# Kernel optimization log

Hardware: AMD Instinct MI355X
Metric: run time of the kernel (lower is better)

Reference implementation:

```python
import jax, jax.numpy as jnp
import numpy as np

B, T, F, G, H, N, C = 32, 64, 32, 32, 256, 20000, 32
EPS = 1e-5


def setup_inputs() -> dict:
    key = jax.random.key(0)
    ks = jax.random.split(key, 24)
    s = 0.05
    d = {}
    d["data_feats"] = jax.random.normal(ks[0], (B, T, F), jnp.float32)
    d["gat_output"] = jax.random.normal(ks[1], (B, N, G), jnp.float32)
    d["row_ids"] = jax.random.randint(ks[2], (B, T), 0, 2 * N, jnp.int32)
    d["node_ids"] = jax.random.randint(ks[3], (N,), 0, 2 * N, jnp.int32)
    # shared LSTM (2 layers): layer0 input F+G, layer1 input H; b = b_ih + b_hh fused
    d["shared_Wih0"] = jax.random.normal(ks[4], (4 * H, F + G)) * s
    d["shared_Whh0"] = jax.random.normal(ks[5], (4 * H, H)) * s
    d["shared_b0"] = jax.random.normal(ks[6], (4 * H,)) * s
    d["shared_Wih1"] = jax.random.normal(ks[7], (4 * H, H)) * s
    d["shared_Whh1"] = jax.random.normal(ks[8], (4 * H, H)) * s
    d["shared_b1"] = jax.random.normal(ks[9], (4 * H,)) * s
    # act/time/timeR LSTMs stacked on leading axis 3, each 2 layers of [4H,H]
    d["heads_Wih"] = jax.random.normal(ks[10], (3, 2, 4 * H, H)) * s
    d["heads_Whh"] = jax.random.normal(ks[11], (3, 2, 4 * H, H)) * s
    d["heads_b"] = jax.random.normal(ks[12], (3, 2, 4 * H)) * s
    d["bn_gnn_g"] = jnp.ones((G,), jnp.float32)
    d["bn_gnn_b"] = jnp.zeros((G,), jnp.float32)
    d["bn_shared_g"] = jnp.ones((H,), jnp.float32)
    d["bn_shared_b"] = jnp.zeros((H,), jnp.float32)
    d["heads_bn_g"] = jnp.ones((3, H), jnp.float32)
    d["heads_bn_b"] = jnp.zeros((3, H), jnp.float32)
    d["fc_act_W"] = jax.random.normal(ks[13], (C, H)) * s
    d["fc_act_b"] = jnp.zeros((C,), jnp.float32)
    d["fc_time_W"] = jax.random.normal(ks[14], (1, H)) * s
    d["fc_time_b"] = jnp.zeros((1,), jnp.float32)
    d["fc_timeR_W"] = jax.random.normal(ks[15], (1, H)) * s
    d["fc_timeR_b"] = jnp.zeros((1,), jnp.float32)
    return d


def batchnorm(x, gamma, beta):
    # BatchNorm1d training-mode: stats over (batch, length) per channel; x: [B, L, C]
    mean = jnp.mean(x, axis=(0, 1))
    var = jnp.var(x, axis=(0, 1))
    return (x - mean) * (gamma / jnp.sqrt(var + EPS)) + beta


def lstm_layer(x, Wih, Whh, b):
    # x: [B, T, Din]; PyTorch gate order i, f, g, o
    xp = jnp.einsum("btf,gf->btg", x, Wih) + b  # [B, T, 4H]
    h = Whh.shape[1]
    init = (jnp.zeros((x.shape[0], h), x.dtype), jnp.zeros((x.shape[0], h), x.dtype))

    def step(carry, xt):
        hprev, cprev = carry
        gates = xt + hprev @ Whh.T
        i, f, g, o = jnp.split(gates, 4, axis=-1)
        c = jax.nn.sigmoid(f) * cprev + jax.nn.sigmoid(i) * jnp.tanh(g)
        hnew = jax.nn.sigmoid(o) * jnp.tanh(c)
        return (hnew, c), hnew

    _, hs = jax.lax.scan(step, init, jnp.swapaxes(xp, 0, 1))
    return jnp.swapaxes(hs, 0, 1)  # [B, T, H]


def reference(data_feats, gat_output, row_ids, node_ids,
              shared_Wih0, shared_Whh0, shared_b0,
              shared_Wih1, shared_Whh1, shared_b1,
              heads_Wih, heads_Whh, heads_b,
              bn_gnn_g, bn_gnn_b, bn_shared_g, bn_shared_b,
              heads_bn_g, heads_bn_b,
              fc_act_W, fc_act_b, fc_time_W, fc_time_b, fc_timeR_W, fc_timeR_b):
    # --- graph branch: BN over GAT output, value-match lookup + gather ---
    gat_norm = batchnorm(gat_output, bn_gnn_g, bn_gnn_b)  # [B, N, G]
    eq = row_ids[:, :, None] == node_ids[None, None, :]   # [B, T, N]
    idx = jnp.argmax(eq, axis=-1)                          # first matching index
    found = jnp.any(eq, axis=-1)
    gathered = jnp.take_along_axis(gat_norm, idx[:, :, None], axis=1)  # [B, T, G]
    matched = jnp.where(found[:, :, None], gathered, 0.0)
    lstm_in = jnp.concatenate([data_feats, matched], axis=-1)  # [B, T, F+G]

    # --- shared 2-layer LSTM + BN (dropout off / eval) ---
    shared = lstm_layer(lstm_in, shared_Wih0, shared_Whh0, shared_b0)
    shared = lstm_layer(shared, shared_Wih1, shared_Whh1, shared_b1)
    shared = batchnorm(shared, bn_shared_g, bn_shared_b)

    # --- act / time / timeR head LSTMs (vmapped over the 3 heads) + BN ---
    def head(Wih, Whh, b, g, bb):
        hh = lstm_layer(shared, Wih[0], Whh[0], b[0])
        hh = lstm_layer(hh, Wih[1], Whh[1], b[1])
        return batchnorm(hh, g, bb)

    heads = jax.vmap(head)(heads_Wih, heads_Whh, heads_b, heads_bn_g, heads_bn_b)
    last = heads[:, :, -1, :]  # [3, B, H]

    act = jax.nn.softmax(last[0] @ fc_act_W.T + fc_act_b, axis=1)
    time = last[1] @ fc_time_W.T + fc_time_b
    timeR = last[2] @ fc_timeR_W.T + fc_timeR_b
    return act, time, timeR
```

## Files before the change

### kernel.cpp

```cpp
#include <hip/hip_runtime.h>
#include <hip/hip_fp16.h>
#include <math.h>

#define Bn 32
#define Tn 64
#define Fdim 32
#define Gdim 32
#define Hdim 256
#define Ndim 20000
#define Cdim 32
#define G4 1024
#define BT 2048
#define EPSc 1e-5f

__device__ __forceinline__ float sigmoidf_(float x){ return 1.0f/(1.0f + __expf(-x)); }
__device__ __forceinline__ float tanhf_(float x){ return 2.0f/(1.0f+__expf(-2.0f*x)) - 1.0f; }

typedef _Float16 h2t __attribute__((ext_vector_type(2)));

__device__ __forceinline__ float fdot2_(unsigned w, unsigned h, float acc){
#if defined(__has_builtin) && __has_builtin(__builtin_amdgcn_fdot2)
  return __builtin_amdgcn_fdot2(__builtin_bit_cast(h2t, w), __builtin_bit_cast(h2t, h), acc, false);
#else
  h2t a = __builtin_bit_cast(h2t, w), b = __builtin_bit_cast(h2t, h);
  acc = fmaf((float)a.x, (float)b.x, acc);
  return fmaf((float)a.y, (float)b.y, acc);
#endif
}

__device__ __forceinline__ unsigned packh_(float lo, float hi){
  unsigned ulo = (unsigned)__half_as_ushort(__float2half(lo));
  unsigned uhi = (unsigned)__half_as_ushort(__float2half(hi));
  return ulo | (uhi << 16);
}

__global__ void init_kernel(float* ws){
  int i = blockIdx.x*256 + threadIdx.x;
  if (i < 2112) ws[i] = 0.0f;
  int* table = (int*)(ws + 2112);
  if (i < 40000) table[i] = 0x7fffffff;
}

__global__ void bn_stats_kernel(const float* __restrict__ gat, float* __restrict__ sums){
  __shared__ float ss[256], sq[256];
  int tid = threadIdx.x;
  int idx = blockIdx.x*256 + tid;
  int stride = gridDim.x*256;
  const int total = Bn*Ndim*Gdim;
  float s=0.f,q=0.f;
  for (int i=idx; i<total; i+=stride){ float v = gat[i]; s+=v; q+=v*v; }
  ss[tid]=s; sq[tid]=q; __syncthreads();
  for (int off=128; off>=32; off>>=1){
    if(tid<off){ ss[tid]+=ss[tid+off]; sq[tid]+=sq[tid+off]; }
    __syncthreads();
  }
  if (tid<32){ atomicAdd(&sums[tid], ss[tid]); atomicAdd(&sums[32+tid], sq[tid]); }
}

__global__ void table_kernel(const int* __restrict__ node_ids, int* __restrict__ table){
  int i = blockIdx.x*256 + threadIdx.x;
  if (i < Ndim) atomicMin(&table[node_ids[i]], i);
}

__global__ void build_input_kernel(const float* __restrict__ feats, const float* __restrict__ gat,
    const int* __restrict__ row_ids, const int* __restrict__ table, const float* __restrict__ sums,
    const float* __restrict__ bng, const float* __restrict__ bnb, unsigned* __restrict__ out){
  int gt = blockIdx.x*256 + threadIdx.x;
  int pos = gt >> 5; int k2 = gt & 31;
  float lo, hi;
  if (k2 < 16){
    float2 v = *(const float2*)(feats + pos*Fdim + 2*k2);
    lo = v.x; hi = v.y;
  } else {
    int g0 = 2*(k2-16);
    int r = row_ids[pos];
    int idx = table[r];
    if (idx < Ndim){
      int b = pos / Tn;
      float2 x = *(const float2*)(gat + (size_t)(b*Ndim + idx)*Gdim + g0);
      const float cnt = (float)(Bn*Ndim);
      float m0 = sums[g0]/cnt,   v0 = sums[32+g0]/cnt - m0*m0;
      float m1 = sums[g0+1]/cnt, v1 = sums[32+g0+1]/cnt - m1*m1;
      lo = (x.x-m0)*bng[g0]*rsqrtf(v0+EPSc) + bnb[g0];
      hi = (x.y-m1)*bng[g0+1]*rsqrtf(v1+EPSc) + bnb[g0+1];
    } else { lo = 0.0f; hi = 0.0f; }
  }
  out[gt] = packh_(lo, hi);
}

struct TArgs { const float* src[8]; unsigned* dst[8]; int K[8]; };
__global__ void packwih_kernel(TArgs a){
  __shared__ unsigned tile[32][33];
  int mat = blockIdx.y;
  int K = a.K[mat];
  int K2 = K >> 1;
  int ktiles = K2 >> 5;
  int tk = blockIdx.x & 3;
  int tn = blockIdx.x >> 2;
  if (tk >= ktiles) return;
  const float* src = a.src[mat];
  unsigned* dst = a.dst[mat];
  int tx = threadIdx.x, ty = threadIdx.y;
  int n0 = tn*32, k2_0 = tk*32;
  #pragma unroll
  for (int i=0;i<4;i++){
    int nn = ty + 8*i;
    const float* p = src + (size_t)(n0+nn)*K + 2*(k2_0 + tx);
    tile[nn][tx] = packh_(p[0], p[1]);
  }
  __syncthreads();
  #pragma unroll
  for (int i=0;i<4;i++){
    int r = ty + 8*i;
    dst[(size_t)(k2_0 + r)*G4 + n0 + tx] = tile[tx][r];
  }
}

struct PkArgs { const float* src[8]; };
__global__ void pack_kernel(PkArgs a, unsigned* __restrict__ dst){
  int gid = blockIdx.x*256 + threadIdx.x;
  int m = gid >> 17;
  int rem = gid & 0x1FFFF;
  int q = rem & 3;
  int t2 = (rem >> 2) & 1023;
  int ci = rem >> 12;
  int c = ci >> 3, i = ci & 7;
  int j = t2 & 255, kq = t2 >> 8;
  int r = 4*j + c;
  int k = kq*64 + 8*i + 2*q;
  const float* W = a.src[m];
  dst[gid] = packh_(W[r*256 + k], W[r*256 + k + 1]);
}

struct PArgs { const unsigned* x[3]; const unsigned* wt[3]; const float* bias[3]; float* out[3]; int K2; };
__global__ __launch_bounds__(256) void proj_kernel(PArgs a){
  int hd = blockIdx.z;
  int n  = blockIdx.y*256 + threadIdx.x;
  int m0 = blockIdx.x*8;
  int K2 = a.K2;
  const unsigned* xh = a.x[hd] + (size_t)m0*K2;
  const unsigned* wt = a.wt[hd];
  float bv = a.bias[hd][n];
  float acc[8];
  #pragma unroll
  for (int i=0;i<8;i++) acc[i]=bv;
  for (int k2=0;k2<K2;k2+=4){
    unsigned w0 = wt[(size_t)(k2+0)*G4+n];
    unsigned w1 = wt[(size_t)(k2+1)*G4+n];
    unsigned w2 = wt[(size_t)(k2+2)*G4+n];
    unsigned w3 = wt[(size_t)(k2+3)*G4+n];
    #pragma unroll
    for (int i=0;i<8;i++){
      uint4 xv = *(const uint4*)(xh + i*K2 + k2);
      acc[i]=fdot2_(w0,xv.x,acc[i]); acc[i]=fdot2_(w1,xv.y,acc[i]);
      acc[i]=fdot2_(w2,xv.z,acc[i]); acc[i]=fdot2_(w3,xv.w,acc[i]);
    }
  }
  float* out = a.out[hd] + (size_t)m0*G4 + n;
  #pragma unroll
  for (int i=0;i<8;i++) out[i*G4]=acc[i];
}

struct RArgs { const float* xp[3]; const unsigned* wt[3]; float* out[3]; unsigned* outh[3]; };
__global__ __launch_bounds__(1024,1) void rec_kernel(RArgs a){
  extern __shared__ float lds[];
  unsigned* lw   = (unsigned*)lds;
  float*    part = lds + 32768;
  unsigned* hp   = (unsigned*)(lds + 36864);
  int b = blockIdx.x, hd = blockIdx.y, tid = threadIdx.x;
  int j = tid & 255, kq = tid >> 8;
  const float* xp = a.xp[hd] + (size_t)b*Tn*G4;
  const unsigned* wt = a.wt[hd];
  float* out = a.out[hd] + (size_t)b*Tn*Hdim;
  unsigned* outh = a.outh[hd] + (size_t)b*Tn*128;

  unsigned w[96];
  #pragma unroll
  for (int c=0;c<4;c++){
    #pragma unroll
    for (int i=0;i<6;i++){
      uint4 v = *(const uint4*)(wt + ((c*8+i)*1024 + tid)*4);
      w[(c*6+i)*4+0]=v.x; w[(c*6+i)*4+1]=v.y; w[(c*6+i)*4+2]=v.z; w[(c*6+i)*4+3]=v.w;
    }
    #pragma unroll
    for (int i=6;i<8;i++){
      uint4 v = *(const uint4*)(wt + ((c*8+i)*1024 + tid)*4);
      *(uint4*)(lw + ((c*2+(i-6))*1024 + tid)*4) = v;
    }
  }
  float cst = 0.0f;
  if (tid < 128){ hp[tid] = 0u; hp[128+tid] = 0u; }
  __syncthreads();

  int p = 0;
  for (int t=0; t<Tn; t++){
    float ac0, ac1, ac2, ac3;
    if (kq == 0){
      float4 xv = *(const float4*)(xp + t*G4 + 4*j);
      ac0=xv.x; ac1=xv.y; ac2=xv.z; ac3=xv.w;
    } else { ac0=0.f; ac1=0.f; ac2=0.f; ac3=0.f; }
    const unsigned* hrow = hp + p*128 + kq*32;
    #pragma unroll
    for (int ic=0; ic<6; ic++){
      uint4 hv = *(const uint4*)(hrow + 4*ic);
      ac0=fdot2_(w[0*24+ic*4+0],hv.x,ac0); ac0=fdot2_(w[0*24+ic*4+1],hv.y,ac0);
      ac0=fdot2_(w[0*24+ic*4+2],hv.z,ac0); ac0=fdot2_(w[0*24+ic*4+3],hv.w,ac0);
      ac1=fdot2_(w[1*24+ic*4+0],hv.x,ac1); ac1=fdot2_(w[1*24+ic*4+1],hv.y,ac1);
      ac1=fdot2_(w[1*24+ic*4+2],hv.z,ac1); ac1=fdot2_(w[1*24+ic*4+3],hv.w,ac1);
      ac2=fdot2_(w[2*24+ic*4+0],hv.x,ac2); ac2=fdot2_(w[2*24+ic*4+1],hv.y,ac2);
      ac2=fdot2_(w[2*24+ic*4+2],hv.z,ac2); ac2=fdot2_(w[2*24+ic*4+3],hv.w,ac2);
      ac3=fdot2_(w[3*24+ic*4+0],hv.x,ac3); ac3=fdot2_(w[3*24+ic*4+1],hv.y,ac3);
      ac3=fdot2_(w[3*24+ic*4+2],hv.z,ac3); ac3=fdot2_(w[3*24+ic*4+3],hv.w,ac3);
    }
    #pragma unroll
    for (int ic=6; ic<8; ic++){
      uint4 hv = *(const uint4*)(hrow + 4*ic);
      { uint4 lv = *(const uint4*)(lw + ((0*2+(ic-6))*1024 + tid)*4);
        ac0=fdot2_(lv.x,hv.x,ac0); ac0=fdot2_(lv.y,hv.y,ac0);
        ac0=fdot2_(lv.z,hv.z,ac0); ac0=fdot2_(lv.w,hv.w,ac0); }
      { uint4 lv = *(const uint4*)(lw + ((1*2+(ic-6))*1024 + tid)*4);
        ac1=fdot2_(lv.x,hv.x,ac1); ac1=fdot2_(lv.y,hv.y,ac1);
        ac1=fdot2_(lv.z,hv.z,ac1); ac1=fdot2_(lv.w,hv.w,ac1); }
      { uint4 lv = *(const uint4*)(lw + ((2*2+(ic-6))*1024 + tid)*4);
        ac2=fdot2_(lv.x,hv.x,ac2); ac2=fdot2_(lv.y,hv.y,ac2);
        ac2=fdot2_(lv.z,hv.z,ac2); ac2=fdot2_(lv.w,hv.w,ac2); }
      { uint4 lv = *(const uint4*)(lw + ((3*2+(ic-6))*1024 + tid)*4);
        ac3=fdot2_(lv.x,hv.x,ac3); ac3=fdot2_(lv.y,hv.y,ac3);
        ac3=fdot2_(lv.z,hv.z,ac3); ac3=fdot2_(lv.w,hv.w,ac3); }
    }
    *(float4*)(part + kq*1024 + 4*j) = make_float4(ac0,ac1,ac2,ac3);
    __syncthreads();
    if (tid < 256){
      int u = tid;
      float gi = part[u]     + part[1024+u]     + part[2048+u]     + part[3072+u];
      float gf = part[256+u] + part[1024+256+u] + part[2048+256+u] + part[3072+256+u];
      float gg = part[512+u] + part[1024+512+u] + part[2048+512+u] + part[3072+512+u];
      float go = part[768+u] + part[1024+768+u] + part[2048+768+u] + part[3072+768+u];
      cst = sigmoidf_(gf)*cst + sigmoidf_(gi)*tanhf_(gg);
      float h = sigmoidf_(go)*tanhf_(cst);
      out[t*Hdim + u] = h;
      float hpartner = __shfl_xor(h, 1);
      if ((u & 1) == 0){
        unsigned hh = packh_(h, hpartner);
        hp[(p^1)*128 + (u>>1)] = hh;
        outh[t*128 + (u>>1)] = hh;
      }
    }
    __syncthreads();
    p ^= 1;
  }
}

struct SArgs { const float* in[3]; float* stats[3]; };
__global__ void stats_kernel(SArgs a){
  int hd = blockIdx.y; int tid = threadIdx.x;
  const float* in = a.in[hd] + blockIdx.x*256*Hdim;
  float s=0.f,q=0.f;
  for (int r=0;r<256;r++){ float v = in[r*Hdim + tid]; s+=v; q+=v*v; }
  atomicAdd(&a.stats[hd][tid], s);
  atomicAdd(&a.stats[hd][Hdim+tid], q);
}

__global__ void norm_kernel(const float* __restrict__ in, const float* __restrict__ stats,
   const float* __restrict__ g, const float* __restrict__ bta, unsigned* __restrict__ outh){
  int i2 = blockIdx.x*256 + threadIdx.x;
  int h2 = i2 & 127; int m = i2 >> 7;
  int h0 = 2*h2;
  float2 v = *(const float2*)(in + (size_t)m*Hdim + h0);
  float m0 = stats[h0]*(1.0f/BT),   v0 = stats[Hdim+h0]*(1.0f/BT) - m0*m0;
  float m1 = stats[h0+1]*(1.0f/BT), v1 = stats[Hdim+h0+1]*(1.0f/BT) - m1*m1;
  float lo = (v.x-m0)*g[h0]*rsqrtf(v0+EPSc) + bta[h0];
  float hi = (v.y-m1)*g[h0+1]*rsqrtf(v1+EPSc) + bta[h0+1];
  outh[i2] = packh_(lo, hi);
}

__global__ __launch_bounds__(256) void final_kernel(
  const float* __restrict__ h0, const float* __restrict__ h1, const float* __restrict__ h2,
  const float* __restrict__ stats,
  const float* __restrict__ hbg, const float* __restrict__ hbb,
  const float* __restrict__ actW, const float* __restrict__ actB,
  const float* __restrict__ tW, const float* __restrict__ tB,
  const float* __restrict__ rW, const float* __restrict__ rB,
  float* __restrict__ outp){
  __shared__ float v0[Bn*Hdim];
  __shared__ float lg[Bn*Cdim];
  int tid = threadIdx.x;
  for (int i=tid; i<Bn*Hdim; i+=256){
    int b=i>>8, h=i&255;
    float sm = stats[512 + h], sq = stats[512+256+h];
    float mean = sm*(1.0f/BT); float var = sq*(1.0f/BT) - mean*mean;
    v0[i] = (h0[(b*Tn+63)*Hdim + h] - mean)*hbg[h]*rsqrtf(var+EPSc) + hbb[h];
  }
  __syncthreads();
  for (int i=tid; i<Bn*Cdim; i+=256){
    int b=i>>5, cc=i&31;
    float acc = actB[cc];
    const float* wrow = actW + cc*Hdim;
    const float* vrow = v0 + b*Hdim;
    #pragma unroll 4
    for (int h=0;h<Hdim;h++) acc = fmaf(vrow[h], wrow[h], acc);
    lg[i] = acc;
  }
  __syncthreads();
  if (tid < Bn){
    int b = tid;
    float m = -1e30f;
    #pragma unroll
    for (int cc=0; cc<Cdim; cc++) m = fmaxf(m, lg[b*Cdim+cc]);
    float e[Cdim]; float s = 0.f;
    #pragma unroll
    for (int cc=0; cc<Cdim; cc++){ float ee = __expf(lg[b*Cdim+cc]-m); e[cc]=ee; s+=ee; }
    float inv = 1.0f/s;
    #pragma unroll
    for (int cc=0; cc<Cdim; cc++) outp[b*Cdim+cc] = e[cc]*inv;
  }
  if (tid < 64){
    int b = tid & 31; int w = tid >> 5;
    const float* hh = w ? h2 : h1;
    const float* fw = w ? rW : tW;
    float fb = w ? rB[0] : tB[0];
    int hd = 1 + w;
    float acc = fb;
    for (int h=0; h<Hdim; h++){
      float sm = stats[(1+hd)*512 + h], sq = stats[(1+hd)*512+256+h];
      float mean = sm*(1.0f/BT); float var = sq*(1.0f/BT) - mean*mean;
      float v = (hh[(b*Tn+63)*Hdim + h] - mean)*hbg[hd*Hdim+h]*rsqrtf(var+EPSc) + hbb[hd*Hdim+h];
      acc = fmaf(v, fw[h], acc);
    }
    outp[1024 + w*32 + b] = acc;
  }
}

extern "C" void kernel_launch(void* const* d_in, const int* in_sizes, int n_in,
                              void* d_out, int out_size, void* d_ws, size_t ws_size,
                              hipStream_t stream){
  const float* data_feats = (const float*)d_in[0];
  const float* gat   = (const float*)d_in[1];
  const int*   row_ids  = (const int*)d_in[2];
  const int*   node_ids = (const int*)d_in[3];
  const float* sWih0 = (const float*)d_in[4];
  const float* sWhh0 = (const float*)d_in[5];
  const float* sb0   = (const float*)d_in[6];
  const float* sWih1 = (const float*)d_in[7];
  const float* sWhh1 = (const float*)d_in[8];
  const float* sb1   = (const float*)d_in[9];
  const float* hWih  = (const float*)d_in[10];
  const float* hWhh  = (const float*)d_in[11];
  const float* hb    = (const float*)d_in[12];
  const float* bng   = (const float*)d_in[13];
  const float* bnb   = (const float*)d_in[14];
  const float* bsg   = (const float*)d_in[15];
  const float* bsb   = (const float*)d_in[16];
  const float* hbg   = (const float*)d_in[17];
  const float* hbb   = (const float*)d_in[18];
  const float* actW  = (const float*)d_in[19];
  const float* actB  = (const float*)d_in[20];
  const float* tW    = (const float*)d_in[21];
  const float* tB    = (const float*)d_in[22];
  const float* rW    = (const float*)d_in[23];
  const float* rB    = (const float*)d_in[24];
  float* ws  = (float*)d_ws;
  float* out = (float*)d_out;

  const size_t S_GAT = 0;
  const size_t S_BN  = 64;
  const size_t TABLE = 2112;
  const size_t WIHP  = 42112;
  const size_t PSLOT = 131072;
  const size_t WHHP  = WIHP + 8*PSLOT;
  const size_t LSTM_INH = WHHP + 8*PSLOT;
  const size_t XPOFF = LSTM_INH + 65536;
  const size_t BUF0H = XPOFF + 3*2097152;
  const size_t BUF1  = BUF0H + 262144;
  const size_t BUFNH = BUF1 + 524288;
  const size_t HB0H  = BUFNH + 262144;
  const size_t HB1   = HB0H + 3*262144;

  const int REC_LDS = 148480;
  hipFuncSetAttribute((const void*)rec_kernel, hipFuncAttributeMaxDynamicSharedMemorySize, REC_LDS);

  init_kernel<<<157,256,0,stream>>>(ws);
  bn_stats_kernel<<<2048,256,0,stream>>>(gat, ws+S_GAT);
  table_kernel<<<(Ndim+255)/256,256,0,stream>>>(node_ids, (int*)(ws+TABLE));
  build_input_kernel<<<256,256,0,stream>>>(data_feats, gat, row_ids, (int*)(ws+TABLE),
                                           ws+S_GAT, bng, bnb, (unsigned*)(ws+LSTM_INH));

  unsigned* wih = (unsigned*)(ws + WIHP);
  TArgs ta;
  ta.src[0]=sWih0; ta.K[0]=64;
  ta.src[1]=sWih1; ta.K[1]=256;
  for (int hd=0; hd<3; hd++) for (int l=0;l<2;l++){
    ta.src[2+hd*2+l] = hWih + (size_t)(hd*2+l)*G4*Hdim; ta.K[2+hd*2+l] = 256;
  }
  for (int i=0;i<8;i++) ta.dst[i] = wih + (size_t)i*PSLOT;
  packwih_kernel<<<dim3(128,8),dim3(32,8),0,stream>>>(ta);

  unsigned* whh = (unsigned*)(ws + WHHP);
  PkArgs pka;
  pka.src[0]=sWhh0; pka.src[1]=sWhh1;
  for (int hd=0; hd<3; hd++) for (int l=0;l<2;l++)
    pka.src[2+hd*2+l] = hWhh + (size_t)(hd*2+l)*G4*Hdim;
  pack_kernel<<<4096,256,0,stream>>>(pka, whh);

  PArgs pa; RArgs ra; SArgs sa;
  pa.K2=32; pa.x[0]=(unsigned*)(ws+LSTM_INH); pa.wt[0]=wih+0*PSLOT; pa.bias[0]=sb0; pa.out[0]=ws+XPOFF;
  proj_kernel<<<dim3(256,4,1),256,0,stream>>>(pa);
  ra.xp[0]=ws+XPOFF; ra.wt[0]=whh+0*PSLOT; ra.out[0]=ws+BUF1;  ra.outh[0]=(unsigned*)(ws+BUF0H);
  rec_kernel<<<dim3(32,1),1024,REC_LDS,stream>>>(ra);
  pa.K2=128; pa.x[0]=(unsigned*)(ws+BUF0H); pa.wt[0]=wih+1*PSLOT; pa.bias[0]=sb1; pa.out[0]=ws+XPOFF;
  proj_kernel<<<dim3(256,4,1),256,0,stream>>>(pa);
  ra.xp[0]=ws+XPOFF; ra.wt[0]=whh+1*PSLOT; ra.out[0]=ws+BUF1; ra.outh[0]=(unsigned*)(ws+BUF0H);
  rec_kernel<<<dim3(32,1),1024,REC_LDS,stream>>>(ra);
  sa.in[0]=ws+BUF1; sa.stats[0]=ws+S_BN;
  stats_kernel<<<dim3(8,1),256,0,stream>>>(sa);
  norm_kernel<<<1024,256,0,stream>>>(ws+BUF1, ws+S_BN, bsg, bsb, (unsigned*)(ws+BUFNH));
  pa.K2=128;
  for (int hd=0;hd<3;hd++){
    pa.x[hd]=(unsigned*)(ws+BUFNH); pa.wt[hd]=wih+(size_t)(2+hd*2)*PSLOT; pa.bias[hd]=hb + (size_t)(hd*2)*G4;
    pa.out[hd]=ws+XPOFF+(size_t)hd*2097152;
  }
  proj_kernel<<<dim3(256,4,3),256,0,stream>>>(pa);
  for (int hd=0;hd<3;hd++){
    ra.xp[hd]=ws+XPOFF+(size_t)hd*2097152; ra.wt[hd]=whh+(size_t)(2+hd*2)*PSLOT;
    ra.out[hd]=ws+HB1+(size_t)hd*524288;  ra.outh[hd]=(unsigned*)(ws+HB0H)+(size_t)hd*262144;
  }
  rec_kernel<<<dim3(32,3),1024,REC_LDS,stream>>>(ra);
  for (int hd=0;hd<3;hd++){
    pa.x[hd]=(unsigned*)(ws+HB0H)+(size_t)hd*262144; pa.wt[hd]=wih+(size_t)(2+hd*2+1)*PSLOT;
    pa.bias[hd]=hb + (size_t)(hd*2+1)*G4;
    pa.out[hd]=ws+XPOFF+(size_t)hd*2097152;
  }
  proj_kernel<<<dim3(256,4,3),256,0,stream>>>(pa);
  for (int hd=0;hd<3;hd++){
    ra.xp[hd]=ws+XPOFF+(size_t)hd*2097152; ra.wt[hd]=whh+(size_t)(2+hd*2+1)*PSLOT;
    ra.out[hd]=ws+HB1+(size_t)hd*524288; ra.outh[hd]=(unsigned*)(ws+HB0H)+(size_t)hd*262144;
  }
  rec_kernel<<<dim3(32,3),1024,REC_LDS,stream>>>(ra);
  for (int hd=0;hd<3;hd++){ sa.in[hd]=ws+HB1+(size_t)hd*524288; sa.stats[hd]=ws+S_BN+(size_t)(1+hd)*512; }
  stats_kernel<<<dim3(8,3),256,0,stream>>>(sa);
  final_kernel<<<1,256,0,stream>>>(ws+HB1, ws+HB1+524288, ws+HB1+2*524288, ws+S_BN,
                                   hbg, hbb, actW, actB, tW, tB, rW, rB, out);
}
```

Before: 865.2 us.

## Reduce LSTM gate partials with DPP quad sums and one barrier per step

The recurrent kernel's thread-to-work mapping changes so the four K-slices of each hidden unit sit in adjacent lanes. Gate partial sums are then reduced with DPP quad shuffles instead of an LDS partials buffer, and every thread computes the cell update redundantly. This drops one of the two block barriers per timestep along with the LDS round trip. The weight packing, the gate column permutation in the W_ih pack and the bias indexing are all remapped to match, and the next step's input projection is prefetched. The hidden-state buffer is padded, and the risk is correctness in the many coupled index permutations.

```diff
diff --git a/kernel.cpp b/kernel.cpp
--- a/kernel.cpp
+++ b/kernel.cpp
@@ -32,6 +32,14 @@
   unsigned ulo = (unsigned)__half_as_ushort(__float2half(lo));
   unsigned uhi = (unsigned)__half_as_ushort(__float2half(hi));
   return ulo | (uhi << 16);
+}
+
+__device__ __forceinline__ float quad_sum_(float x){
+  int a = __builtin_amdgcn_mov_dpp(__builtin_bit_cast(int,x), 0xB1, 0xF, 0xF, true);
+  x += __builtin_bit_cast(float,a);
+  int b = __builtin_amdgcn_mov_dpp(__builtin_bit_cast(int,x), 0x4E, 0xF, 0xF, true);
+  x += __builtin_bit_cast(float,b);
+  return x;
 }
 
 __global__ void init_kernel(float* ws){
@@ -109,10 +117,12 @@
     tile[nn][tx] = packh_(p[0], p[1]);
   }
   __syncthreads();
+  int col = n0 + tx;
+  int pcol = 4*(col & 255) + (col >> 8);
   #pragma unroll
   for (int i=0;i<4;i++){
     int r = ty + 8*i;
-    dst[(size_t)(k2_0 + r)*G4 + n0 + tx] = tile[tx][r];
+    dst[(size_t)(k2_0 + r)*G4 + pcol] = tile[tx][r];
   }
 }
 
@@ -120,14 +130,13 @@
 __global__ void pack_kernel(PkArgs a, unsigned* __restrict__ dst){
   int gid = blockIdx.x*256 + threadIdx.x;
   int m = gid >> 17;
-  int rem = gid & 0x1FFFF;
-  int q = rem & 3;
-  int t2 = (rem >> 2) & 1023;
-  int ci = rem >> 12;
-  int c = ci >> 3, i = ci & 7;
-  int j = t2 & 255, kq = t2 >> 8;
-  int r = 4*j + c;
-  int k = kq*64 + 8*i + 2*q;
+  int dd = gid & 0x1FFFF;
+  int d = dd & 3;
+  int tid = (dd >> 2) & 1023;
+  int ce = dd >> 12;
+  int c = ce >> 3, e = ce & 7;
+  int r = c*256 + 16*(tid>>6) + ((tid>>2)&15);
+  int k = 64*(tid & 3) + 8*e + 2*d;
   const float* W = a.src[m];
   dst[gid] = packh_(W[r*256 + k], W[r*256 + k + 1]);
 }
@@ -140,7 +149,7 @@
   int K2 = a.K2;
   const unsigned* xh = a.x[hd] + (size_t)m0*K2;
   const unsigned* wt = a.wt[hd];
-  float bv = a.bias[hd][n];
+  float bv = a.bias[hd][(n & 3)*256 + (n >> 2)];
   float acc[8];
   #pragma unroll
   for (int i=0;i<8;i++) acc[i]=bv;
@@ -164,11 +173,12 @@
 struct RArgs { const float* xp[3]; const unsigned* wt[3]; float* out[3]; unsigned* outh[3]; };
 __global__ __launch_bounds__(1024,1) void rec_kernel(RArgs a){
   extern __shared__ float lds[];
-  unsigned* lw   = (unsigned*)lds;
-  float*    part = lds + 32768;
-  unsigned* hp   = (unsigned*)(lds + 36864);
+  unsigned* lw = (unsigned*)lds;
+  unsigned* hp = (unsigned*)lds + 32768;
   int b = blockIdx.x, hd = blockIdx.y, tid = threadIdx.x;
-  int j = tid & 255, kq = tid >> 8;
+  int ks = tid & 3;
+  bool ks0 = (ks == 0);
+  int unit = 16*(tid>>6) + ((tid>>2)&15);
   const float* xp = a.xp[hd] + (size_t)b*Tn*G4;
   const unsigned* wt = a.wt[hd];
   float* out = a.out[hd] + (size_t)b*Tn*Hdim;
@@ -188,66 +198,65 @@
       *(uint4*)(lw + ((c*2+(i-6))*1024 + tid)*4) = v;
     }
   }
+  if (tid < 288){ hp[tid] = 0u; }
   float cst = 0.0f;
-  if (tid < 128){ hp[tid] = 0u; hp[128+tid] = 0u; }
+  float4 xc = *(const float4*)(xp + 4*unit);
   __syncthreads();
 
   int p = 0;
   for (int t=0; t<Tn; t++){
-    float ac0, ac1, ac2, ac3;
-    if (kq == 0){
-      float4 xv = *(const float4*)(xp + t*G4 + 4*j);
-      ac0=xv.x; ac1=xv.y; ac2=xv.z; ac3=xv.w;
-    } else { ac0=0.f; ac1=0.f; ac2=0.f; ac3=0.f; }
-    const unsigned* hrow = hp + p*128 + kq*32;
-    #pragma unroll
-    for (int ic=0; ic<6; ic++){
-      uint4 hv = *(const uint4*)(hrow + 4*ic);
-      ac0=fdot2_(w[0*24+ic*4+0],hv.x,ac0); ac0=fdot2_(w[0*24+ic*4+1],hv.y,ac0);
-      ac0=fdot2_(w[0*24+ic*4+2],hv.z,ac0); ac0=fdot2_(w[0*24+ic*4+3],hv.w,ac0);
-      ac1=fdot2_(w[1*24+ic*4+0],hv.x,ac1); ac1=fdot2_(w[1*24+ic*4+1],hv.y,ac1);
-      ac1=fdot2_(w[1*24+ic*4+2],hv.z,ac1); ac1=fdot2_(w[1*24+ic*4+3],hv.w,ac1);
-      ac2=fdot2_(w[2*24+ic*4+0],hv.x,ac2); ac2=fdot2_(w[2*24+ic*4+1],hv.y,ac2);
-      ac2=fdot2_(w[2*24+ic*4+2],hv.z,ac2); ac2=fdot2_(w[2*24+ic*4+3],hv.w,ac2);
-      ac3=fdot2_(w[3*24+ic*4+0],hv.x,ac3); ac3=fdot2_(w[3*24+ic*4+1],hv.y,ac3);
-      ac3=fdot2_(w[3*24+ic*4+2],hv.z,ac3); ac3=fdot2_(w[3*24+ic*4+3],hv.w,ac3);
-    }
-    #pragma unroll
-    for (int ic=6; ic<8; ic++){
-      uint4 hv = *(const uint4*)(hrow + 4*ic);
-      { uint4 lv = *(const uint4*)(lw + ((0*2+(ic-6))*1024 + tid)*4);
+    float4 xn = *(const float4*)(xp + (size_t)(t+1)*G4 + 4*unit);
+    const unsigned* hq = hp + p*144 + ks*36;
+    float ac0 = ks0 ? xc.x : 0.0f;
+    float ac1 = ks0 ? xc.y : 0.0f;
+    float ac2 = ks0 ? xc.z : 0.0f;
+    float ac3 = ks0 ? xc.w : 0.0f;
+    #pragma unroll
+    for (int e=0;e<6;e++){
+      uint4 hv = *(const uint4*)(hq + 4*e);
+      ac0=fdot2_(w[(0*6+e)*4+0],hv.x,ac0); ac0=fdot2_(w[(0*6+e)*4+1],hv.y,ac0);
+      ac0=fdot2_(w[(0*6+e)*4+2],hv.z,ac0); ac0=fdot2_(w[(0*6+e)*4+3],hv.w,ac0);
+      ac1=fdot2_(w[(1*6+e)*4+0],hv.x,ac1); ac1=fdot2_(w[(1*6+e)*4+1],hv.y,ac1);
+      ac1=fdot2_(w[(1*6+e)*4+2],hv.z,ac1); ac1=fdot2_(w[(1*6+e)*4+3],hv.w,ac1);
+      ac2=fdot2_(w[(2*6+e)*4+0],hv.x,ac2); ac2=fdot2_(w[(2*6+e)*4+1],hv.y,ac2);
+      ac2=fdot2_(w[(2*6+e)*4+2],hv.z,ac2); ac2=fdot2_(w[(2*6+e)*4+3],hv.w,ac2);
+      ac3=fdot2_(w[(3*6+e)*4+0],hv.x,ac3); ac3=fdot2_(w[(3*6+e)*4+1],hv.y,ac3);
+      ac3=fdot2_(w[(3*6+e)*4+2],hv.z,ac3); ac3=fdot2_(w[(3*6+e)*4+3],hv.w,ac3);
+    }
+    #pragma unroll
+    for (int e=6;e<8;e++){
+      uint4 hv = *(const uint4*)(hq + 4*e);
+      { uint4 lv = *(const uint4*)(lw + ((0*2+(e-6))*1024 + tid)*4);
         ac0=fdot2_(lv.x,hv.x,ac0); ac0=fdot2_(lv.y,hv.y,ac0);
         ac0=fdot2_(lv.z,hv.z,ac0); ac0=fdot2_(lv.w,hv.w,ac0); }
-      { uint4 lv = *(const uint4*)(lw + ((1*2+(ic-6))*1024 + tid)*4);
+      { uint4 lv = *(const uint4*)(lw + ((1*2+(e-6))*1024 + tid)*4);
         ac1=fdot2_(lv.x,hv.x,ac1); ac1=fdot2_(lv.y,hv.y,ac1);
         ac1=fdot2_(lv.z,hv.z,ac1); ac1=fdot2_(lv.w,hv.w,ac1); }
-      { uint4 lv = *(const uint4*)(lw + ((2*2+(ic-6))*1024 + tid)*4);
+      { uint4 lv = *(const uint4*)(lw + ((2*2+(e-6))*1024 + tid)*4);
         ac2=fdot2_(lv.x,hv.x,ac2); ac2=fdot2_(lv.y,hv.y,ac2);
         ac2=fdot2_(lv.z,hv.z,ac2); ac2=fdot2_(lv.w,hv.w,ac2); }
-      { uint4 lv = *(const uint4*)(lw + ((3*2+(ic-6))*1024 + tid)*4);
+      { uint4 lv = *(const uint4*)(lw + ((3*2+(e-6))*1024 + tid)*4);
         ac3=fdot2_(lv.x,hv.x,ac3); ac3=fdot2_(lv.y,hv.y,ac3);
         ac3=fdot2_(lv.z,hv.z,ac3); ac3=fdot2_(lv.w,hv.w,ac3); }
     }
-    *(float4*)(part + kq*1024 + 4*j) = make_float4(ac0,ac1,ac2,ac3);
-    __syncthreads();
-    if (tid < 256){
-      int u = tid;
-      float gi = part[u]     + part[1024+u]     + part[2048+u]     + part[3072+u];
-      float gf = part[256+u] + part[1024+256+u] + part[2048+256+u] + part[3072+256+u];
-      float gg = part[512+u] + part[1024+512+u] + part[2048+512+u] + part[3072+512+u];
-      float go = part[768+u] + part[1024+768+u] + part[2048+768+u] + part[3072+768+u];
-      cst = sigmoidf_(gf)*cst + sigmoidf_(gi)*tanhf_(gg);
-      float h = sigmoidf_(go)*tanhf_(cst);
-      out[t*Hdim + u] = h;
-      float hpartner = __shfl_xor(h, 1);
-      if ((u & 1) == 0){
-        unsigned hh = packh_(h, hpartner);
-        hp[(p^1)*128 + (u>>1)] = hh;
-        outh[t*128 + (u>>1)] = hh;
-      }
-    }
-    __syncthreads();
+    ac0 = quad_sum_(ac0);
+    ac1 = quad_sum_(ac1);
+    ac2 = quad_sum_(ac2);
+    ac3 = quad_sum_(ac3);
+    cst = sigmoidf_(ac1)*cst + sigmoidf_(ac0)*tanhf_(ac2);
+    float h = sigmoidf_(ac3)*tanhf_(cst);
+    float hpart = __shfl_xor(h, 4);
+    if (ks0) out[t*Hdim + unit] = h;
+    if ((tid & 7) == 0){
+      unsigned hh = packh_(h, hpart);
+      int m = 8*(tid>>6) + ((tid>>3)&7);
+      hp[(p^1)*144 + (m>>5)*36 + (m&31)] = hh;
+      outh[t*128 + m] = hh;
+    }
+    asm volatile("s_waitcnt lgkmcnt(0)" ::: "memory");
+    __builtin_amdgcn_s_barrier();
     p ^= 1;
+    xc = xn;
   }
 }
 
@@ -376,7 +385,7 @@
   const size_t HB0H  = BUFNH + 262144;
   const size_t HB1   = HB0H + 3*262144;
 
-  const int REC_LDS = 148480;
+  const int REC_LDS = 132224;
   hipFuncSetAttribute((const void*)rec_kernel, hipFuncAttributeMaxDynamicSharedMemorySize, REC_LDS);
 
   init_kernel<<<157,256,0,stream>>>(ws);
```

Result: slower. 963.4 us (+11.3%).
